# Kernel optimization log

Measured on AMD Instinct MI355X. Metric: run time of the kernel, lower is better.

Reference implementation:

```python
import jax, jax.numpy as jnp
import numpy as np

B, S, D, H = 4, 2048, 1024, 16
HD = D // H
LN_EPS = 1e-5


def _layer_norm(x, g, b):
    mu = jnp.mean(x, axis=-1, keepdims=True)
    var = jnp.mean(jnp.square(x - mu), axis=-1, keepdims=True)
    return (x - mu) * jax.lax.rsqrt(var + LN_EPS) * g + b


def setup_inputs() -> dict:
    key = jax.random.key(0)
    ks = jax.random.split(key, 8)
    sd = 1.0 / np.sqrt(D)
    return {
        "features": jax.random.normal(ks[0], (B, S, D), dtype=jnp.float32),
        "in_proj_w": jax.random.uniform(ks[1], (3 * D, D), jnp.float32, -sd, sd),
        "in_proj_b": jnp.zeros((3 * D,), jnp.float32),
        "out_proj_w": jax.random.uniform(ks[2], (D, D), jnp.float32, -sd, sd),
        "out_proj_b": jnp.zeros((D,), jnp.float32),
        "ln_g": jnp.ones((D,), jnp.float32),
        "ln_b": jnp.zeros((D,), jnp.float32),
        "w1": jax.random.uniform(ks[3], (2 * D, D), jnp.float32, -sd, sd),
        "b1": jax.random.uniform(ks[4], (2 * D,), jnp.float32, -sd, sd),
        "w2": jax.random.uniform(ks[5], (D, 2 * D), jnp.float32, -1.0 / np.sqrt(2 * D), 1.0 / np.sqrt(2 * D)),
        "b2": jax.random.uniform(ks[6], (D,), jnp.float32, -1.0 / np.sqrt(2 * D), 1.0 / np.sqrt(2 * D)),
    }


def reference(features, in_proj_w, in_proj_b, out_proj_w, out_proj_b, ln_g, ln_b, w1, b1, w2, b2):
    x = features  # [B,S,D]
    qkv = x @ in_proj_w.T + in_proj_b  # [B,S,3D]
    q, k, v = jnp.split(qkv, 3, axis=-1)
    # [B,H,S,hd]
    q = q.reshape(B, S, H, HD).transpose(0, 2, 1, 3)
    k = k.reshape(B, S, H, HD).transpose(0, 2, 1, 3)
    v = v.reshape(B, S, H, HD).transpose(0, 2, 1, 3)
    scores = jnp.einsum("bhqd,bhkd->bhqk", q, k) / np.sqrt(HD).astype(np.float32)
    attn = jax.nn.softmax(scores, axis=-1)  # [B,H,S,S]
    ctx = jnp.einsum("bhqk,bhkd->bhqd", attn, v)  # [B,H,S,hd]
    ctx = ctx.transpose(0, 2, 1, 3).reshape(B, S, D)
    attended = ctx @ out_proj_w.T + out_proj_b
    # torch MHA default: average attention weights over heads
    attn_weights = jnp.mean(attn, axis=1)  # [B,S,S]
    h = _layer_norm(attended + x, ln_g, ln_b)
    ff = jax.nn.gelu(h @ w1.T + b1, approximate=False) @ w2.T + b2  # dropout = identity (eval)
    out = _layer_norm(ff + h, ln_g, ln_b)
    return (out, attn_weights)
```

## Files before the change

### kernel.cpp

```cpp
#include <hip/hip_runtime.h>
#include <hip/hip_bf16.h>
#include <math.h>

#define B_ 4
#define S_ 2048
#define D_ 1024
#define H_ 16
#define HD_ 64
#define TRIPLE 3072

typedef __attribute__((ext_vector_type(8))) short bf16x8;
typedef __attribute__((ext_vector_type(4))) float f32x4;
typedef __attribute__((ext_vector_type(8))) unsigned short u16x8;
typedef unsigned short ushort_t;

#define MFMA(a, b, c) __builtin_amdgcn_mfma_f32_16x16x32_bf16((a), (b), (c), 0, 0, 0)

__device__ __forceinline__ ushort_t f2bf(float f) {
    union { float f; unsigned int u; } u; u.f = f;
    unsigned int r = u.u + 0x7fff + ((u.u >> 16) & 1);
    return (ushort_t)(r >> 16);
}
__device__ __forceinline__ float bf2f(ushort_t h) {
    union { unsigned int u; float f; } u; u.u = ((unsigned int)h) << 16;
    return u.f;
}

__global__ __launch_bounds__(256) void castk(const float* __restrict__ s,
                                             ushort_t* __restrict__ d, int n) {
    int i = (blockIdx.x * 256 + threadIdx.x) * 8;
    if (i >= n) return;
    float4 a = *(const float4*)(s + i);
    float4 b = *(const float4*)(s + i + 4);
    u16x8 o;
    o[0] = f2bf(a.x); o[1] = f2bf(a.y); o[2] = f2bf(a.z); o[3] = f2bf(a.w);
    o[4] = f2bf(b.x); o[5] = f2bf(b.y); o[6] = f2bf(b.z); o[7] = f2bf(b.w);
    *(u16x8*)(d + i) = o;
}

__global__ __launch_bounds__(256) void gemm_bf16(
    const ushort_t* __restrict__ A, const ushort_t* __restrict__ W,
    const float* __restrict__ bias, ushort_t* __restrict__ C,
    int N, int K, int act)
{
    __shared__ char Asb[128 * 128];
    __shared__ char Wsb[128 * 128];
    const int tid = threadIdx.x;
    const int wv = tid >> 6, lane = tid & 63;
    const int fr = lane & 15, fq = lane >> 4;
    const int wr = wv >> 1, wc = wv & 1;
    const int m0 = blockIdx.y * 128, n0 = blockIdx.x * 128;
    const int srow = tid >> 1, sh = tid & 1;

    const ushort_t* Ag = A + (size_t)(m0 + srow) * K + sh * 32;
    const ushort_t* Wg = W + (size_t)(n0 + srow) * K + sh * 32;
    const int swb = srow * 128;
    const int sxr = srow & 7;
    const int fx = fr & 7;

    const f32x4 fz = {0.f, 0.f, 0.f, 0.f};
    f32x4 acc[4][4];
    #pragma unroll
    for (int i = 0; i < 4; ++i)
        #pragma unroll
        for (int j = 0; j < 4; ++j) acc[i][j] = fz;

    for (int k0 = 0; k0 < K; k0 += 64) {
        u16x8 av[4], wvv[4];
        #pragma unroll
        for (int c = 0; c < 4; ++c) {
            av[c] = *(const u16x8*)(Ag + k0 + c * 8);
            wvv[c] = *(const u16x8*)(Wg + k0 + c * 8);
        }
        __syncthreads();
        #pragma unroll
        for (int c = 0; c < 4; ++c) {
            int slot = (sh * 4 + c) ^ sxr;
            *(u16x8*)(Asb + swb + slot * 16) = av[c];
            *(u16x8*)(Wsb + swb + slot * 16) = wvv[c];
        }
        __syncthreads();
        #pragma unroll
        for (int ks = 0; ks < 2; ++ks) {
            bf16x8 af[4], bfr[4];
            #pragma unroll
            for (int i = 0; i < 4; ++i) {
                int ra = wr * 64 + i * 16 + fr;
                int rb = wc * 64 + i * 16 + fr;
                int slot = (ks * 4 + fq) ^ fx;
                af[i] = *(const bf16x8*)(Asb + ra * 128 + slot * 16);
                bfr[i] = *(const bf16x8*)(Wsb + rb * 128 + slot * 16);
            }
            #pragma unroll
            for (int i = 0; i < 4; ++i)
                #pragma unroll
                for (int j = 0; j < 4; ++j)
                    acc[i][j] = MFMA(af[i], bfr[j], acc[i][j]);
        }
    }

    float bv[4];
    #pragma unroll
    for (int j = 0; j < 4; ++j) bv[j] = bias[n0 + wc * 64 + j * 16 + fr];
    #pragma unroll
    for (int i = 0; i < 4; ++i) {
        #pragma unroll
        for (int j = 0; j < 4; ++j) {
            int col = n0 + wc * 64 + j * 16 + fr;
            #pragma unroll
            for (int r = 0; r < 4; ++r) {
                int row = m0 + wr * 64 + i * 16 + fq * 4 + r;
                float v = acc[i][j][r] + bv[j];
                if (act) v = 0.5f * v * (1.0f + erff(v * 0.70710678118654752f));
                C[(size_t)row * N + col] = f2bf(v);
            }
        }
    }
}

__global__ __launch_bounds__(256) void vtrans(const ushort_t* __restrict__ qkvb,
                                              ushort_t* __restrict__ vT)
{
    __shared__ ushort_t T[64][72];
    const int tid = threadIdx.x;
    const int bh = blockIdx.y;
    const int b = bh >> 4, h = bh & 15;
    const int s0 = blockIdx.x * 64;
    const int r = tid >> 2, q = tid & 3;
    const ushort_t* src = qkvb + (size_t)(b * S_ + s0 + r) * TRIPLE + 2048 + h * 64 + q * 16;
    *(u16x8*)&T[r][q * 16] = *(const u16x8*)(src);
    *(u16x8*)&T[r][q * 16 + 8] = *(const u16x8*)(src + 8);
    __syncthreads();
    u16x8 o0, o1;
    #pragma unroll
    for (int i = 0; i < 8; ++i) o0[i] = T[q * 16 + i][r];
    #pragma unroll
    for (int i = 0; i < 8; ++i) o1[i] = T[q * 16 + 8 + i][r];
    ushort_t* dstp = vT + ((size_t)bh * 64 + r) * S_ + s0 + q * 16;
    *(u16x8*)(dstp) = o0;
    *(u16x8*)(dstp + 8) = o1;
}

__global__ __launch_bounds__(256) void attn_ctx_mfma(
    const ushort_t* __restrict__ qkvb, const ushort_t* __restrict__ vT,
    ushort_t* __restrict__ ctxb, float* __restrict__ mstat, float* __restrict__ lstat)
{
    __shared__ char Kl[64 * 128];
    __shared__ char Vl[64 * 128];
    __shared__ char Pl[64 * 128];
    const int tid = threadIdx.x;
    const int wv = tid >> 6, lane = tid & 63;
    const int fr = lane & 15, fq = lane >> 4;
    const int fx = fr & 7;
    const int bh = blockIdx.y, b = bh >> 4, h = bh & 15;
    const int q0 = blockIdx.x * 64;

    bf16x8 qf[2];
    {
        const ushort_t* qp = qkvb + (size_t)(b * S_ + q0 + wv * 16 + fr) * TRIPLE + h * 64 + fq * 8;
        qf[0] = *(const bf16x8*)(qp);
        qf[1] = *(const bf16x8*)(qp + 32);
    }

    const int srow = tid >> 2, sq = tid & 3;
    const ushort_t* Kg = qkvb + (size_t)(b * S_ + srow) * TRIPLE + 1024 + h * 64 + sq * 16;
    const ushort_t* Vg = vT + ((size_t)bh * 64 + srow) * S_ + sq * 16;
    const int sb = srow * 128, sxr = srow & 7;
    const int slot0 = (sq * 2) ^ sxr, slot1 = (sq * 2 + 1) ^ sxr;

    const f32x4 fz = {0.f, 0.f, 0.f, 0.f};
    float m_[4], l_[4];
    f32x4 po[4];
    #pragma unroll
    for (int r = 0; r < 4; ++r) { m_[r] = -1e30f; l_[r] = 0.f; }
    #pragma unroll
    for (int dn = 0; dn < 4; ++dn) po[dn] = fz;

    for (int k0 = 0; k0 < S_; k0 += 64) {
        u16x8 ks0 = *(const u16x8*)(Kg + (size_t)k0 * TRIPLE);
        u16x8 ks1 = *(const u16x8*)(Kg + (size_t)k0 * TRIPLE + 8);
        u16x8 vs0 = *(const u16x8*)(Vg + k0);
        u16x8 vs1 = *(const u16x8*)(Vg + k0 + 8);
        __syncthreads();
        *(u16x8*)(Kl + sb + slot0 * 16) = ks0;
        *(u16x8*)(Kl + sb + slot1 * 16) = ks1;
        *(u16x8*)(Vl + sb + slot0 * 16) = vs0;
        *(u16x8*)(Vl + sb + slot1 * 16) = vs1;
        __syncthreads();

        f32x4 sa[4];
        #pragma unroll
        for (int jn = 0; jn < 4; ++jn) sa[jn] = fz;
        #pragma unroll
        for (int ks = 0; ks < 2; ++ks) {
            #pragma unroll
            for (int jn = 0; jn < 4; ++jn) {
                int kr = jn * 16 + fr;
                bf16x8 kf = *(const bf16x8*)(Kl + kr * 128 + (((ks * 4 + fq) ^ fx) * 16));
                sa[jn] = MFMA(qf[ks], kf, sa[jn]);
            }
        }

        float p[4][4], al[4];
        #pragma unroll
        for (int r = 0; r < 4; ++r) {
            float s0v = sa[0][r] * 0.125f, s1v = sa[1][r] * 0.125f;
            float s2v = sa[2][r] * 0.125f, s3v = sa[3][r] * 0.125f;
            float tm = fmaxf(fmaxf(s0v, s1v), fmaxf(s2v, s3v));
            tm = fmaxf(tm, __shfl_xor(tm, 1));
            tm = fmaxf(tm, __shfl_xor(tm, 2));
            tm = fmaxf(tm, __shfl_xor(tm, 4));
            tm = fmaxf(tm, __shfl_xor(tm, 8));
            float mn = fmaxf(m_[r], tm);
            al[r] = __expf(m_[r] - mn);
            p[0][r] = __expf(s0v - mn); p[1][r] = __expf(s1v - mn);
            p[2][r] = __expf(s2v - mn); p[3][r] = __expf(s3v - mn);
            float rs = p[0][r] + p[1][r] + p[2][r] + p[3][r];
            rs += __shfl_xor(rs, 1); rs += __shfl_xor(rs, 2);
            rs += __shfl_xor(rs, 4); rs += __shfl_xor(rs, 8);
            l_[r] = l_[r] * al[r] + rs;
            m_[r] = mn;
        }
        #pragma unroll
        for (int dn = 0; dn < 4; ++dn)
            #pragma unroll
            for (int r = 0; r < 4; ++r) po[dn][r] *= al[r];

        #pragma unroll
        for (int jn = 0; jn < 4; ++jn) {
            int kvslot = jn * 2 + (fr >> 3);
            #pragma unroll
            for (int r = 0; r < 4; ++r) {
                int qq = wv * 16 + fq * 4 + r;
                *(ushort_t*)(Pl + qq * 128 + ((kvslot ^ (qq & 7)) << 4) + (fr & 7) * 2) = f2bf(p[jn][r]);
            }
        }

        const int qrow = wv * 16 + fr;
        #pragma unroll
        for (int ks = 0; ks < 2; ++ks) {
            bf16x8 pf = *(const bf16x8*)(Pl + qrow * 128 + (((ks * 4 + fq) ^ fx) * 16));
            #pragma unroll
            for (int dn = 0; dn < 4; ++dn) {
                int dr = dn * 16 + fr;
                bf16x8 vf = *(const bf16x8*)(Vl + dr * 128 + (((ks * 4 + fq) ^ fx) * 16));
                po[dn] = MFMA(pf, vf, po[dn]);
            }
        }
    }

    if (fr == 0) {
        #pragma unroll
        for (int r = 0; r < 4; ++r) {
            size_t idx = (size_t)bh * S_ + q0 + wv * 16 + fq * 4 + r;
            mstat[idx] = m_[r];
            lstat[idx] = l_[r];
        }
    }
    float inv[4];
    #pragma unroll
    for (int r = 0; r < 4; ++r) inv[r] = 1.0f / l_[r];
    #pragma unroll
    for (int dn = 0; dn < 4; ++dn) {
        int col = h * 64 + dn * 16 + fr;
        #pragma unroll
        for (int r = 0; r < 4; ++r) {
            int row = q0 + wv * 16 + fq * 4 + r;
            ctxb[(size_t)(b * S_ + row) * D_ + col] = f2bf(po[dn][r] * inv[r]);
        }
    }
}

__global__ __launch_bounds__(256) void attn_wts_mfma(
    const ushort_t* __restrict__ qkvb, const float* __restrict__ mstat,
    const float* __restrict__ lstat, float* __restrict__ attnw)
{
    __shared__ char Ql[64 * 128];
    __shared__ char Kl[64 * 128];
    const int tid = threadIdx.x;
    const int wv = tid >> 6, lane = tid & 63;
    const int fr = lane & 15, fq = lane >> 4;
    const int fx = fr & 7;
    const int b = blockIdx.z;
    const int q0 = blockIdx.y * 64, k0 = blockIdx.x * 64;
    const int srow = tid >> 2, sq = tid & 3;
    const int sb = srow * 128, sxr = srow & 7;
    const int slot0 = (sq * 2) ^ sxr, slot1 = (sq * 2 + 1) ^ sxr;

    const f32x4 fz = {0.f, 0.f, 0.f, 0.f};
    float wacc[4][4];
    #pragma unroll
    for (int jn = 0; jn < 4; ++jn)
        #pragma unroll
        for (int r = 0; r < 4; ++r) wacc[jn][r] = 0.f;

    for (int h = 0; h < H_; ++h) {
        const ushort_t* Qg = qkvb + (size_t)(b * S_ + q0 + srow) * TRIPLE + h * 64 + sq * 16;
        const ushort_t* Kg = qkvb + (size_t)(b * S_ + k0 + srow) * TRIPLE + 1024 + h * 64 + sq * 16;
        u16x8 qv0 = *(const u16x8*)(Qg);
        u16x8 qv1 = *(const u16x8*)(Qg + 8);
        u16x8 kv0 = *(const u16x8*)(Kg);
        u16x8 kv1 = *(const u16x8*)(Kg + 8);
        __syncthreads();
        *(u16x8*)(Ql + sb + slot0 * 16) = qv0;
        *(u16x8*)(Ql + sb + slot1 * 16) = qv1;
        *(u16x8*)(Kl + sb + slot0 * 16) = kv0;
        *(u16x8*)(Kl + sb + slot1 * 16) = kv1;
        __syncthreads();

        f32x4 sa[4];
        #pragma unroll
        for (int jn = 0; jn < 4; ++jn) sa[jn] = fz;
        const int qrow = wv * 16 + fr;
        #pragma unroll
        for (int ks = 0; ks < 2; ++ks) {
            bf16x8 qfr = *(const bf16x8*)(Ql + qrow * 128 + (((ks * 4 + fq) ^ fx) * 16));
            #pragma unroll
            for (int jn = 0; jn < 4; ++jn) {
                int kr = jn * 16 + fr;
                bf16x8 kf = *(const bf16x8*)(Kl + kr * 128 + (((ks * 4 + fq) ^ fx) * 16));
                sa[jn] = MFMA(qfr, kf, sa[jn]);
            }
        }

        const float* mp = mstat + (size_t)(b * H_ + h) * S_ + q0 + wv * 16 + fq * 4;
        const float* lp = lstat + (size_t)(b * H_ + h) * S_ + q0 + wv * 16 + fq * 4;
        #pragma unroll
        for (int r = 0; r < 4; ++r) {
            float mi = mp[r], il = 1.0f / lp[r];
            #pragma unroll
            for (int jn = 0; jn < 4; ++jn)
                wacc[jn][r] += __expf(sa[jn][r] * 0.125f - mi) * il;
        }
    }

    #pragma unroll
    for (int jn = 0; jn < 4; ++jn) {
        #pragma unroll
        for (int r = 0; r < 4; ++r) {
            int row = q0 + wv * 16 + fq * 4 + r;
            attnw[(size_t)b * S_ * S_ + (size_t)row * S_ + k0 + jn * 16 + fr] =
                wacc[jn][r] * 0.0625f;
        }
    }
}

__global__ __launch_bounds__(256) void ln_kernel(
    const ushort_t* __restrict__ xin_bf, const float* __restrict__ resid,
    const float* __restrict__ g, const float* __restrict__ bb,
    float* __restrict__ out_f32, ushort_t* __restrict__ out_bf, int write_bf)
{
    const int row = blockIdx.x, tid = threadIdx.x;
    const size_t off = (size_t)row * D_ + tid * 4;
    union { uint2 u2; ushort_t hx[4]; } uu;
    uu.u2 = *(const uint2*)(xin_bf + off);
    float4 rr = *(const float4*)(resid + off);
    float v[4];
    v[0] = bf2f(uu.hx[0]) + rr.x; v[1] = bf2f(uu.hx[1]) + rr.y;
    v[2] = bf2f(uu.hx[2]) + rr.z; v[3] = bf2f(uu.hx[3]) + rr.w;
    float sum = v[0] + v[1] + v[2] + v[3];
    float ssq = v[0]*v[0] + v[1]*v[1] + v[2]*v[2] + v[3]*v[3];
    #pragma unroll
    for (int msk = 1; msk < 64; msk <<= 1) {
        sum += __shfl_xor(sum, msk);
        ssq += __shfl_xor(ssq, msk);
    }
    __shared__ float red[8];
    const int wvi = tid >> 6, ln_ = tid & 63;
    if (ln_ == 0) { red[wvi] = sum; red[4 + wvi] = ssq; }
    __syncthreads();
    sum = red[0] + red[1] + red[2] + red[3];
    ssq = red[4] + red[5] + red[6] + red[7];
    const float mu = sum * (1.0f / D_);
    const float var = ssq * (1.0f / D_) - mu * mu;
    const float rstd = rsqrtf(var + 1e-5f);
    float4 gv = *(const float4*)(g + tid * 4);
    float4 bv = *(const float4*)(bb + tid * 4);
    float o0 = (v[0] - mu) * rstd * gv.x + bv.x;
    float o1 = (v[1] - mu) * rstd * gv.y + bv.y;
    float o2 = (v[2] - mu) * rstd * gv.z + bv.z;
    float o3 = (v[3] - mu) * rstd * gv.w + bv.w;
    *(float4*)(out_f32 + off) = make_float4(o0, o1, o2, o3);
    if (write_bf) {
        union { uint2 u2; ushort_t hx[4]; } ob;
        ob.hx[0] = f2bf(o0); ob.hx[1] = f2bf(o1);
        ob.hx[2] = f2bf(o2); ob.hx[3] = f2bf(o3);
        *(uint2*)(out_bf + off) = ob.u2;
    }
}

extern "C" void kernel_launch(void* const* d_in, const int* in_sizes, int n_in,
                              void* d_out, int out_size, void* d_ws, size_t ws_size,
                              hipStream_t stream)
{
    (void)in_sizes; (void)n_in; (void)out_size; (void)ws_size;
    const float* x    = (const float*)d_in[0];
    const float* wqkv = (const float*)d_in[1];
    const float* bqkv = (const float*)d_in[2];
    const float* wo   = (const float*)d_in[3];
    const float* bo   = (const float*)d_in[4];
    const float* lng  = (const float*)d_in[5];
    const float* lnb  = (const float*)d_in[6];
    const float* w1   = (const float*)d_in[7];
    const float* b1   = (const float*)d_in[8];
    const float* w2   = (const float*)d_in[9];
    const float* b2   = (const float*)d_in[10];

    float* outp  = (float*)d_out;
    float* attnw = outp + (size_t)B_ * S_ * D_;

    char* wsb = (char*)d_ws;
    ushort_t* qkvb  = (ushort_t*)(wsb);
    ushort_t* vT    = (ushort_t*)(wsb + ((size_t)48 << 20));
    ushort_t* ff2b  = vT;
    ushort_t* ctxb  = (ushort_t*)(wsb + ((size_t)64 << 20));
    ushort_t* attdb = (ushort_t*)(wsb + ((size_t)80 << 20));
    float*    hf    = (float*)(wsb + ((size_t)96 << 20));
    ushort_t* hbf   = (ushort_t*)(wsb + ((size_t)128 << 20));
    ushort_t* xb    = (ushort_t*)(wsb + ((size_t)144 << 20));
    ushort_t* ff1b  = xb;
    ushort_t* wqkvb = (ushort_t*)(wsb + ((size_t)176 << 20));
    ushort_t* wob   = (ushort_t*)(wsb + ((size_t)182 << 20));
    ushort_t* w1b   = (ushort_t*)(wsb + ((size_t)184 << 20));
    ushort_t* w2b   = (ushort_t*)(wsb + ((size_t)188 << 20));
    float*    mst   = (float*)(wsb + ((size_t)192 << 20));
    float*    lst   = (float*)(wsb + ((size_t)192 << 20) + ((size_t)512 << 10));

    dim3 blk(256);

    castk<<<dim3(8388608 / 2048), blk, 0, stream>>>(x, xb, 8388608);
    castk<<<dim3(3145728 / 2048), blk, 0, stream>>>(wqkv, wqkvb, 3145728);
    castk<<<dim3(1048576 / 2048), blk, 0, stream>>>(wo, wob, 1048576);
    castk<<<dim3(2097152 / 2048), blk, 0, stream>>>(w1, w1b, 2097152);
    castk<<<dim3(2097152 / 2048), blk, 0, stream>>>(w2, w2b, 2097152);

    gemm_bf16<<<dim3(24, 64), blk, 0, stream>>>(xb, wqkvb, bqkv, qkvb, 3072, 1024, 0);
    vtrans<<<dim3(32, 64), blk, 0, stream>>>(qkvb, vT);
    attn_ctx_mfma<<<dim3(32, 64), blk, 0, stream>>>(qkvb, vT, ctxb, mst, lst);
    attn_wts_mfma<<<dim3(32, 32, 4), blk, 0, stream>>>(qkvb, mst, lst, attnw);
    gemm_bf16<<<dim3(8, 64), blk, 0, stream>>>(ctxb, wob, bo, attdb, 1024, 1024, 0);
    ln_kernel<<<dim3(8192), blk, 0, stream>>>(attdb, x, lng, lnb, hf, hbf, 1);
    gemm_bf16<<<dim3(16, 64), blk, 0, stream>>>(hbf, w1b, b1, ff1b, 2048, 1024, 1);
    gemm_bf16<<<dim3(8, 64), blk, 0, stream>>>(ff1b, w2b, b2, ff2b, 1024, 2048, 0);
    ln_kernel<<<dim3(8192), blk, 0, stream>>>(ff2b, hf, lng, lnb, outp, (ushort_t*)0, 0);
}
```

Before: 725.9 us.

## Use direct global-to-LDS loads in GEMM and transpose attention score layout

```diff
diff --git a/kernel.cpp b/kernel.cpp
--- a/kernel.cpp
+++ b/kernel.cpp
@@ -24,6 +24,13 @@
 __device__ __forceinline__ float bf2f(ushort_t h) {
     union { unsigned int u; float f; } u; u.u = ((unsigned int)h) << 16;
     return u.f;
+}
+
+__device__ __forceinline__ void gload16(const ushort_t* g, void* l) {
+    __builtin_amdgcn_global_load_lds(
+        (const __attribute__((address_space(1))) unsigned int*)g,
+        (__attribute__((address_space(3))) unsigned int*)l,
+        16, 0, 0);
 }
 
 __global__ __launch_bounds__(256) void castk(const float* __restrict__ s,
@@ -50,13 +57,11 @@
     const int fr = lane & 15, fq = lane >> 4;
     const int wr = wv >> 1, wc = wv & 1;
     const int m0 = blockIdx.y * 128, n0 = blockIdx.x * 128;
-    const int srow = tid >> 1, sh = tid & 1;
-
-    const ushort_t* Ag = A + (size_t)(m0 + srow) * K + sh * 32;
-    const ushort_t* Wg = W + (size_t)(n0 + srow) * K + sh * 32;
-    const int swb = srow * 128;
-    const int sxr = srow & 7;
-    const int fx = fr & 7;
+
+    const int lrow = lane >> 3;
+    const int lke  = (lane & 7) * 8;
+    const ushort_t* Agl = A + (size_t)(m0 + wv * 32 + lrow) * K + lke;
+    const ushort_t* Wgl = W + (size_t)(n0 + wv * 32 + lrow) * K + lke;
 
     const f32x4 fz = {0.f, 0.f, 0.f, 0.f};
     f32x4 acc[4][4];
@@ -66,18 +71,11 @@
         for (int j = 0; j < 4; ++j) acc[i][j] = fz;
 
     for (int k0 = 0; k0 < K; k0 += 64) {
-        u16x8 av[4], wvv[4];
+        __syncthreads();
         #pragma unroll
         for (int c = 0; c < 4; ++c) {
-            av[c] = *(const u16x8*)(Ag + k0 + c * 8);
-            wvv[c] = *(const u16x8*)(Wg + k0 + c * 8);
-        }
-        __syncthreads();
-        #pragma unroll
-        for (int c = 0; c < 4; ++c) {
-            int slot = (sh * 4 + c) ^ sxr;
-            *(u16x8*)(Asb + swb + slot * 16) = av[c];
-            *(u16x8*)(Wsb + swb + slot * 16) = wvv[c];
+            gload16(Agl + k0 + c * 8 * K, Asb + (wv * 32 + c * 8) * 128);
+            gload16(Wgl + k0 + c * 8 * K, Wsb + (wv * 32 + c * 8) * 128);
         }
         __syncthreads();
         #pragma unroll
@@ -85,11 +83,8 @@
             bf16x8 af[4], bfr[4];
             #pragma unroll
             for (int i = 0; i < 4; ++i) {
-                int ra = wr * 64 + i * 16 + fr;
-                int rb = wc * 64 + i * 16 + fr;
-                int slot = (ks * 4 + fq) ^ fx;
-                af[i] = *(const bf16x8*)(Asb + ra * 128 + slot * 16);
-                bfr[i] = *(const bf16x8*)(Wsb + rb * 128 + slot * 16);
+                af[i]  = *(const bf16x8*)(Asb + (wr * 64 + i * 16 + fr) * 128 + (ks * 4 + fq) * 16);
+                bfr[i] = *(const bf16x8*)(Wsb + (wc * 64 + i * 16 + fr) * 128 + (ks * 4 + fq) * 16);
             }
             #pragma unroll
             for (int i = 0; i < 4; ++i)
@@ -154,10 +149,11 @@
     const int fx = fr & 7;
     const int bh = blockIdx.y, b = bh >> 4, h = bh & 15;
     const int q0 = blockIdx.x * 64;
+    const int q = wv * 16 + fr;
 
     bf16x8 qf[2];
     {
-        const ushort_t* qp = qkvb + (size_t)(b * S_ + q0 + wv * 16 + fr) * TRIPLE + h * 64 + fq * 8;
+        const ushort_t* qp = qkvb + (size_t)(b * S_ + q0 + q) * TRIPLE + h * 64 + fq * 8;
         qf[0] = *(const bf16x8*)(qp);
         qf[1] = *(const bf16x8*)(qp + 32);
     }
@@ -169,10 +165,8 @@
     const int slot0 = (sq * 2) ^ sxr, slot1 = (sq * 2 + 1) ^ sxr;
 
     const f32x4 fz = {0.f, 0.f, 0.f, 0.f};
-    float m_[4], l_[4];
+    float m_ = -1e30f, l_ = 0.f;
     f32x4 po[4];
-    #pragma unroll
-    for (int r = 0; r < 4; ++r) { m_[r] = -1e30f; l_[r] = 0.f; }
     #pragma unroll
     for (int dn = 0; dn < 4; ++dn) po[dn] = fz;
 
@@ -197,49 +191,58 @@
             for (int jn = 0; jn < 4; ++jn) {
                 int kr = jn * 16 + fr;
                 bf16x8 kf = *(const bf16x8*)(Kl + kr * 128 + (((ks * 4 + fq) ^ fx) * 16));
-                sa[jn] = MFMA(qf[ks], kf, sa[jn]);
-            }
-        }
-
-        float p[4][4], al[4];
-        #pragma unroll
-        for (int r = 0; r < 4; ++r) {
-            float s0v = sa[0][r] * 0.125f, s1v = sa[1][r] * 0.125f;
-            float s2v = sa[2][r] * 0.125f, s3v = sa[3][r] * 0.125f;
-            float tm = fmaxf(fmaxf(s0v, s1v), fmaxf(s2v, s3v));
-            tm = fmaxf(tm, __shfl_xor(tm, 1));
-            tm = fmaxf(tm, __shfl_xor(tm, 2));
-            tm = fmaxf(tm, __shfl_xor(tm, 4));
-            tm = fmaxf(tm, __shfl_xor(tm, 8));
-            float mn = fmaxf(m_[r], tm);
-            al[r] = __expf(m_[r] - mn);
-            p[0][r] = __expf(s0v - mn); p[1][r] = __expf(s1v - mn);
-            p[2][r] = __expf(s2v - mn); p[3][r] = __expf(s3v - mn);
-            float rs = p[0][r] + p[1][r] + p[2][r] + p[3][r];
-            rs += __shfl_xor(rs, 1); rs += __shfl_xor(rs, 2);
-            rs += __shfl_xor(rs, 4); rs += __shfl_xor(rs, 8);
-            l_[r] = l_[r] * al[r] + rs;
-            m_[r] = mn;
-        }
-        #pragma unroll
-        for (int dn = 0; dn < 4; ++dn)
-            #pragma unroll
-            for (int r = 0; r < 4; ++r) po[dn][r] *= al[r];
+                sa[jn] = MFMA(kf, qf[ks], sa[jn]);
+            }
+        }
+
+        float pmax = sa[0][0];
+        #pragma unroll
+        for (int jn = 0; jn < 4; ++jn)
+            #pragma unroll
+            for (int r = 0; r < 4; ++r) pmax = fmaxf(pmax, sa[jn][r]);
+        pmax *= 0.125f;
+        pmax = fmaxf(pmax, __shfl_xor(pmax, 16));
+        pmax = fmaxf(pmax, __shfl_xor(pmax, 32));
+
+        if (!__all(pmax - m_ <= 8.0f)) {
+            float mn = fmaxf(m_, pmax);
+            float al = __expf(m_ - mn);
+            m_ = mn; l_ *= al;
+            float alr[4];
+            #pragma unroll
+            for (int r = 0; r < 4; ++r) alr[r] = __shfl(al, fq * 4 + r);
+            #pragma unroll
+            for (int dn = 0; dn < 4; ++dn)
+                #pragma unroll
+                for (int r = 0; r < 4; ++r) po[dn][r] *= alr[r];
+        }
+
+        float p[4][4];
+        float rs = 0.f;
+        #pragma unroll
+        for (int jn = 0; jn < 4; ++jn)
+            #pragma unroll
+            for (int r = 0; r < 4; ++r) {
+                p[jn][r] = __expf(fmaf(sa[jn][r], 0.125f, -m_));
+                rs += p[jn][r];
+            }
+        rs += __shfl_xor(rs, 16);
+        rs += __shfl_xor(rs, 32);
+        l_ += rs;
 
         #pragma unroll
         for (int jn = 0; jn < 4; ++jn) {
-            int kvslot = jn * 2 + (fr >> 3);
-            #pragma unroll
-            for (int r = 0; r < 4; ++r) {
-                int qq = wv * 16 + fq * 4 + r;
-                *(ushort_t*)(Pl + qq * 128 + ((kvslot ^ (qq & 7)) << 4) + (fr & 7) * 2) = f2bf(p[jn][r]);
-            }
-        }
-
-        const int qrow = wv * 16 + fr;
+            unsigned pk0, pk1;
+            asm("v_cvt_pk_bf16_f32 %0, %1, %2" : "=v"(pk0) : "v"(p[jn][0]), "v"(p[jn][1]));
+            asm("v_cvt_pk_bf16_f32 %0, %1, %2" : "=v"(pk1) : "v"(p[jn][2]), "v"(p[jn][3]));
+            int slot = (jn * 2 + (fq >> 1)) ^ fx;
+            uint2 pw; pw.x = pk0; pw.y = pk1;
+            *(uint2*)(Pl + q * 128 + slot * 16 + (fq & 1) * 8) = pw;
+        }
+
         #pragma unroll
         for (int ks = 0; ks < 2; ++ks) {
-            bf16x8 pf = *(const bf16x8*)(Pl + qrow * 128 + (((ks * 4 + fq) ^ fx) * 16));
+            bf16x8 pf = *(const bf16x8*)(Pl + q * 128 + (((ks * 4 + fq) ^ fx) * 16));
             #pragma unroll
             for (int dn = 0; dn < 4; ++dn) {
                 int dr = dn * 16 + fr;
@@ -249,17 +252,16 @@
         }
     }
 
-    if (fr == 0) {
-        #pragma unroll
-        for (int r = 0; r < 4; ++r) {
-            size_t idx = (size_t)bh * S_ + q0 + wv * 16 + fq * 4 + r;
-            mstat[idx] = m_[r];
-            lstat[idx] = l_[r];
-        }
+    if (fq == 0) {
+        mstat[(size_t)bh * S_ + q0 + q] = m_;
+        lstat[(size_t)bh * S_ + q0 + q] = l_;
     }
     float inv[4];
-    #pragma unroll
-    for (int r = 0; r < 4; ++r) inv[r] = 1.0f / l_[r];
+    {
+        float il = 1.0f / l_;
+        #pragma unroll
+        for (int r = 0; r < 4; ++r) inv[r] = __shfl(il, fq * 4 + r);
+    }
     #pragma unroll
     for (int dn = 0; dn < 4; ++dn) {
         int col = h * 64 + dn * 16 + fr;
@@ -286,6 +288,7 @@
     const int srow = tid >> 2, sq = tid & 3;
     const int sb = srow * 128, sxr = srow & 7;
     const int slot0 = (sq * 2) ^ sxr, slot1 = (sq * 2 + 1) ^ sxr;
+    const int q = wv * 16 + fr;
 
     const f32x4 fz = {0.f, 0.f, 0.f, 0.f};
     float wacc[4][4];
@@ -311,37 +314,32 @@
         f32x4 sa[4];
         #pragma unroll
         for (int jn = 0; jn < 4; ++jn) sa[jn] = fz;
-        const int qrow = wv * 16 + fr;
         #pragma unroll
         for (int ks = 0; ks < 2; ++ks) {
-            bf16x8 qfr = *(const bf16x8*)(Ql + qrow * 128 + (((ks * 4 + fq) ^ fx) * 16));
+            bf16x8 qfr = *(const bf16x8*)(Ql + q * 128 + (((ks * 4 + fq) ^ fx) * 16));
             #pragma unroll
             for (int jn = 0; jn < 4; ++jn) {
                 int kr = jn * 16 + fr;
                 bf16x8 kf = *(const bf16x8*)(Kl + kr * 128 + (((ks * 4 + fq) ^ fx) * 16));
-                sa[jn] = MFMA(qfr, kf, sa[jn]);
-            }
-        }
-
-        const float* mp = mstat + (size_t)(b * H_ + h) * S_ + q0 + wv * 16 + fq * 4;
-        const float* lp = lstat + (size_t)(b * H_ + h) * S_ + q0 + wv * 16 + fq * 4;
-        #pragma unroll
-        for (int r = 0; r < 4; ++r) {
-            float mi = mp[r], il = 1.0f / lp[r];
-            #pragma unroll
-            for (int jn = 0; jn < 4; ++jn)
-                wacc[jn][r] += __expf(sa[jn][r] * 0.125f - mi) * il;
-        }
-    }
-
+                sa[jn] = MFMA(kf, qfr, sa[jn]);
+            }
+        }
+
+        const float mi = mstat[(size_t)(b * H_ + h) * S_ + q0 + q];
+        const float il = 1.0f / lstat[(size_t)(b * H_ + h) * S_ + q0 + q];
+        #pragma unroll
+        for (int jn = 0; jn < 4; ++jn)
+            #pragma unroll
+            for (int r = 0; r < 4; ++r)
+                wacc[jn][r] += __expf(fmaf(sa[jn][r], 0.125f, -mi)) * il;
+    }
+
+    float* dst = attnw + (size_t)b * S_ * S_ + (size_t)(q0 + q) * S_ + k0;
     #pragma unroll
     for (int jn = 0; jn < 4; ++jn) {
-        #pragma unroll
-        for (int r = 0; r < 4; ++r) {
-            int row = q0 + wv * 16 + fq * 4 + r;
-            attnw[(size_t)b * S_ * S_ + (size_t)row * S_ + k0 + jn * 16 + fr] =
-                wacc[jn][r] * 0.0625f;
-        }
+        float4 v = make_float4(wacc[jn][0] * 0.0625f, wacc[jn][1] * 0.0625f,
+                               wacc[jn][2] * 0.0625f, wacc[jn][3] * 0.0625f);
+        *(float4*)(dst + jn * 16 + fq * 4) = v;
     }
 }
 
```

New measurement: 728.7 us. About the same (+0.4%).
